# Kernel tuning notes

Measured on AMD Instinct MI355X. Metric: run time of the kernel, lower is better.

The kernel has to match this reference:

```python
import jax, jax.numpy as jnp
import numpy as np

N_NODES = 100000
N_EDGES = 1600000
D_FEAT = 64


def setup_inputs() -> dict:
    key = jax.random.key(0)
    k1, k2 = jax.random.split(key)
    x = jax.random.normal(k1, (N_NODES, D_FEAT), dtype=jnp.float32)
    edge_index = jax.random.randint(k2, (2, N_EDGES), 0, N_NODES, dtype=jnp.int64)
    alpha = jnp.ones((), dtype=jnp.float32)
    res_scale = jnp.ones((), dtype=jnp.float32)
    return {"x": x, "alpha": alpha, "res_scale": res_scale, "edge_index": edge_index}


def reference(x, alpha, res_scale, edge_index):
    """LGConv (symmetric gcn_norm, no self-loops) -> alpha-scale -> residual.

    out_i = alpha * sum_{(j->i) in E} x_j / sqrt(deg_i * deg_j) + res_scale * x_i
    """
    n = x.shape[0]
    row, col = edge_index[0], edge_index[1]  # source, target
    # degree from target index (as in PyG gcn_norm with add_self_loops=False)
    deg = jax.ops.segment_sum(jnp.ones(row.shape[0], dtype=x.dtype), col, num_segments=n)
    deg_inv_sqrt = jnp.where(deg > 0, jax.lax.rsqrt(jnp.maximum(deg, 1.0)), 0.0)
    norm = deg_inv_sqrt[row] * deg_inv_sqrt[col]  # (E,)
    msgs = norm[:, None] * x[row]                  # (E, d) gather + scale
    out = jax.ops.segment_sum(msgs, col, num_segments=n)  # scatter-add to targets
    return alpha * out + res_scale * x
```

## Files before the change

### kernel.cpp

```cpp
#include <hip/hip_runtime.h>
#include <hip/hip_bf16.h>

#define D_FEAT 64
#define OVF_CAP 65536
#define EB 8192
#define NBMAX 1024

typedef unsigned int uint32;

__device__ inline float blo(uint32 u) { return __uint_as_float(u << 16); }
__device__ inline float bhi(uint32 u) { return __uint_as_float(u & 0xffff0000u); }
__device__ inline float dinv(int d) { return (d > 0) ? rsqrtf((float)d) : 0.0f; }
__device__ inline uint32 pack_bf16x2(float a, float b) {
    __hip_bfloat16 ba = __float2bfloat16(a);
    __hip_bfloat16 bb = __float2bfloat16(b);
    uint32 ua = *reinterpret_cast<unsigned short*>(&ba);
    uint32 ub = *reinterpret_cast<unsigned short*>(&bb);
    return ua | (ub << 16);
}

__global__ __launch_bounds__(256) void k_hist(const int* __restrict__ col,
                                              int* __restrict__ histT,
                                              int E, int B, int nb) {
    __shared__ int h[NBMAX];
    for (int i = threadIdx.x; i < nb; i += 256) h[i] = 0;
    __syncthreads();
    const int b = blockIdx.x;
    const int s = b * EB;
    const int e = (s + EB < E) ? s + EB : E;
    for (int i = s + threadIdx.x; i < e; i += 256)
        atomicAdd(&h[col[i] >> 8], 1);
    __syncthreads();
    for (int k = threadIdx.x; k < nb; k += 256)
        histT[(size_t)k * B + b] = h[k];
}

__global__ __launch_bounds__(512) void k_colscan(int* __restrict__ histT,
                                                 int* __restrict__ total, int B) {
    __shared__ int sh[512];
    const int k = blockIdx.x;
    int v = (threadIdx.x < B) ? histT[(size_t)k * B + threadIdx.x] : 0;
    sh[threadIdx.x] = v;
    __syncthreads();
    for (int off = 1; off < 512; off <<= 1) {
        int t = (threadIdx.x >= off) ? sh[threadIdx.x - off] : 0;
        __syncthreads();
        sh[threadIdx.x] += t;
        __syncthreads();
    }
    int incl = sh[threadIdx.x];
    if (threadIdx.x < B) histT[(size_t)k * B + threadIdx.x] = incl - v;
    if (threadIdx.x == 511) total[k] = incl;
}

__global__ __launch_bounds__(1024) void k_tinyscan(const int* __restrict__ total,
                                                   int* __restrict__ bstart,
                                                   int* __restrict__ ovf_cnt, int nb) {
    __shared__ int sh[1024];
    int v = (threadIdx.x < nb) ? total[threadIdx.x] : 0;
    sh[threadIdx.x] = v;
    __syncthreads();
    for (int off = 1; off < 1024; off <<= 1) {
        int t = (threadIdx.x >= off) ? sh[threadIdx.x - off] : 0;
        __syncthreads();
        sh[threadIdx.x] += t;
        __syncthreads();
    }
    if (threadIdx.x < nb) bstart[threadIdx.x] = sh[threadIdx.x] - v;
    if (threadIdx.x == nb - 1) bstart[nb] = sh[threadIdx.x];
    if (threadIdx.x == 1023) *ovf_cnt = 0;
}

__global__ __launch_bounds__(256) void k_scat3(const int* __restrict__ row,
                                               const int* __restrict__ col,
                                               const int* __restrict__ histT,
                                               const int* __restrict__ bstart,
                                               uint32* __restrict__ binned,
                                               int E, int B, int nb) {
    __shared__ int cur[NBMAX];
    const int b = blockIdx.x;
    for (int k = threadIdx.x; k < nb; k += 256)
        cur[k] = bstart[k] + histT[(size_t)k * B + b];
    __syncthreads();
    const int s = b * EB;
    const int e = (s + EB < E) ? s + EB : E;
    for (int i = s + threadIdx.x; i < e; i += 256) {
        int c = col[i];
        uint32 r = (uint32)row[i];
        int pos = atomicAdd(&cur[c >> 8], 1);
        binned[pos] = (r << 8) | (uint32)(c & 255);
    }
}

__global__ __launch_bounds__(1024) void k_build(const int* __restrict__ bstart,
                                                const uint32* __restrict__ binned,
                                                const float2* __restrict__ x2,
                                                int* __restrict__ slots,
                                                int* __restrict__ deg,
                                                uint32* __restrict__ xb,
                                                int2* __restrict__ ovf,
                                                int* __restrict__ ovf_cnt,
                                                int n, int C) {
    __shared__ int cnt[256];
    __shared__ float sw[256];
    const int k = blockIdx.x;
    if (threadIdx.x < 256) cnt[threadIdx.x] = 0;
    __syncthreads();
    const int s = bstart[k], e = bstart[k + 1];
    const int base = k << 8;
    for (int i = s + threadIdx.x; i < e; i += 1024) {
        uint32 pk = binned[i];
        int cl = (int)(pk & 255);
        int r  = (int)(pk >> 8);
        int rk = atomicAdd(&cnt[cl], 1);
        int c  = base + cl;
        if (rk < C) {
            slots[(size_t)c * C + rk] = r;
        } else {
            int o = atomicAdd(ovf_cnt, 1);
            if (o < OVF_CAP) ovf[o] = make_int2(r, c);
        }
    }
    __syncthreads();
    if (threadIdx.x < 256) {
        int i = base + threadIdx.x;
        int d = cnt[threadIdx.x];
        sw[threadIdx.x] = dinv(d);
        if (i < n) deg[i] = d;
    }
    __syncthreads();
    for (int idx = threadIdx.x; idx < 256 * 32; idx += 1024) {
        int nl = idx >> 5;
        int i  = base + nl;
        if (i >= n) break;
        float w = sw[nl];
        float2 v = x2[(size_t)i * 32 + (idx & 31)];
        xb[(size_t)i * 32 + (idx & 31)] = pack_bf16x2(v.x * w, v.y * w);
    }
}

__global__ void k_gather2(const uint32* __restrict__ xb,
                          const float4* __restrict__ x4,
                          const int* __restrict__ deg,
                          const int* __restrict__ slots,
                          const float* __restrict__ alpha_p,
                          const float* __restrict__ rs_p,
                          float4* __restrict__ out4, int n, int C) {
    int wave = (blockIdx.x * blockDim.x + threadIdx.x) >> 6;
    const int lane = threadIdx.x & 63;
    const int half = lane >> 5;
    const int hl   = lane & 31;
    const int q    = hl >> 3;
    const int l    = hl & 7;
    int wid = wave * 2 + half;
    bool active = (wid < n);
    int d = active ? deg[wid] : 0;
    int e = (d < C) ? d : C;
    const int* sl = slots + (size_t)wid * C;
    float a0 = 0.f, a1 = 0.f, a2 = 0.f, a3 = 0.f;
    float a4 = 0.f, a5 = 0.f, a6 = 0.f, a7 = 0.f;
    for (int k = 0; k < e; k += 8) {
        int k1 = k + q;
        int k2 = k + 4 + q;
        if (k1 < e) {
            int s0 = sl[k1];
            uint4 p = ((const uint4*)(xb + (size_t)s0 * 32))[l];
            a0 += blo(p.x); a1 += bhi(p.x); a2 += blo(p.y); a3 += bhi(p.y);
            a4 += blo(p.z); a5 += bhi(p.z); a6 += blo(p.w); a7 += bhi(p.w);
        }
        if (k2 < e) {
            int s1 = sl[k2];
            uint4 p = ((const uint4*)(xb + (size_t)s1 * 32))[l];
            a0 += blo(p.x); a1 += bhi(p.x); a2 += blo(p.y); a3 += bhi(p.y);
            a4 += blo(p.z); a5 += bhi(p.z); a6 += blo(p.w); a7 += bhi(p.w);
        }
    }
    a0 += __shfl_down(a0, 16, 64); a1 += __shfl_down(a1, 16, 64);
    a2 += __shfl_down(a2, 16, 64); a3 += __shfl_down(a3, 16, 64);
    a4 += __shfl_down(a4, 16, 64); a5 += __shfl_down(a5, 16, 64);
    a6 += __shfl_down(a6, 16, 64); a7 += __shfl_down(a7, 16, 64);
    a0 += __shfl_down(a0, 8, 64);  a1 += __shfl_down(a1, 8, 64);
    a2 += __shfl_down(a2, 8, 64);  a3 += __shfl_down(a3, 8, 64);
    a4 += __shfl_down(a4, 8, 64);  a5 += __shfl_down(a5, 8, 64);
    a6 += __shfl_down(a6, 8, 64);  a7 += __shfl_down(a7, 8, 64);
    if (q == 0 && active) {
        float adw = (*alpha_p) * dinv(d);
        float rs  = *rs_p;
        size_t base = (size_t)wid * 16 + 2 * l;
        float4 xr0 = x4[base];
        float4 xr1 = x4[base + 1];
        float4 o0, o1;
        o0.x = fmaf(adw, a0, rs * xr0.x);
        o0.y = fmaf(adw, a1, rs * xr0.y);
        o0.z = fmaf(adw, a2, rs * xr0.z);
        o0.w = fmaf(adw, a3, rs * xr0.w);
        o1.x = fmaf(adw, a4, rs * xr1.x);
        o1.y = fmaf(adw, a5, rs * xr1.y);
        o1.z = fmaf(adw, a6, rs * xr1.z);
        o1.w = fmaf(adw, a7, rs * xr1.w);
        out4[base]     = o0;
        out4[base + 1] = o1;
    }
}

__global__ void k_ovf(const int2* __restrict__ ovf, const int* __restrict__ cnt_p,
                      const float* __restrict__ x, const int* __restrict__ deg,
                      const float* __restrict__ alpha_p, float* __restrict__ out) {
    int cnt = *cnt_p;
    if (cnt > OVF_CAP) cnt = OVF_CAP;
    if (cnt <= 0) return;
    float a = *alpha_p;
    long long total = (long long)cnt * 64;
    long long stride = (long long)gridDim.x * blockDim.x;
    for (long long idx = blockIdx.x * (long long)blockDim.x + threadIdx.x;
         idx < total; idx += stride) {
        int e = (int)(idx >> 6);
        int f = (int)(idx & 63);
        int2 rc = ovf[e];
        float w = a * dinv(deg[rc.x]) * dinv(deg[rc.y]);
        atomicAdd(&out[(size_t)rc.y * D_FEAT + f], w * x[(size_t)rc.x * D_FEAT + f]);
    }
}

__global__ void k_prep(const int* __restrict__ row, const int* __restrict__ col,
                       int* __restrict__ deg, int* __restrict__ slots,
                       int2* __restrict__ ovf, int* __restrict__ ovf_cnt,
                       int E, int C) {
    int t = blockIdx.x * blockDim.x + threadIdx.x;
    if (t < E) {
        int c = col[t];
        int r = row[t];
        int rk = atomicAdd(&deg[c], 1);
        if (rk < C) {
            slots[(size_t)c * C + rk] = r;
        } else {
            int o = atomicAdd(ovf_cnt, 1);
            if (o < OVF_CAP) ovf[o] = make_int2(r, c);
        }
    }
}
__global__ void k_cast(const float2* __restrict__ x2, const int* __restrict__ deg,
                       uint32* __restrict__ xb, int nhalf) {
    int t = blockIdx.x * blockDim.x + threadIdx.x;
    if (t < nhalf) {
        float w = dinv(deg[t >> 5]);
        float2 v = x2[t];
        xb[t] = pack_bf16x2(v.x * w, v.y * w);
    }
}

static inline char* align_up(char* p, size_t a) {
    return (char*)(((uintptr_t)p + (a - 1)) & ~(uintptr_t)(a - 1));
}

extern "C" void kernel_launch(void* const* d_in, const int* in_sizes, int n_in,
                              void* d_out, int out_size, void* d_ws, size_t ws_size,
                              hipStream_t stream) {
    const float* x         = (const float*)d_in[0];
    const float* alpha     = (const float*)d_in[1];
    const float* res_scale = (const float*)d_in[2];
    const int*   ei        = (const int*)d_in[3];

    const int n = in_sizes[0] / D_FEAT;
    const int E = in_sizes[3] / 2;
    const int* row = ei;
    const int* col = ei + E;

    float* out = (float*)d_out;
    const int nhalf = n * (D_FEAT / 2);
    const int nb = (n + 255) >> 8;
    const int B  = (E + EB - 1) / EB;

    const int nwaves = (n + 1) / 2;
    const int gblocks = (nwaves * 64 + 255) / 256;

    {
        char* p = (char*)d_ws;
        int*    deg     = (int*)p;            p += (size_t)n * 4;
        int*    ovf_cnt = (int*)p;            p += 4;
        int2*   ovf     = (int2*)p;           p += (size_t)OVF_CAP * 8;
        int*    histT   = (int*)p;            p += (size_t)nb * B * 4;
        int*    total   = (int*)p;            p += (size_t)nb * 4;
        int*    bstart  = (int*)p;            p += (size_t)(nb + 1) * 4;
        p = align_up(p, 16);
        uint32* xb      = (uint32*)p;         p += (size_t)n * 128;
        uint32* binned  = (uint32*)p;         p += (size_t)E * 4;
        int*    slots   = (int*)p;
        const size_t fixed = (size_t)(p - (char*)d_ws);

        int C = 0;
        if (ws_size > fixed) {
            size_t c_avail = (ws_size - fixed) / ((size_t)n * 4);
            C = (c_avail > 32) ? 32 : (int)c_avail;
        }
        const bool ok = (C >= 16) && (nb <= NBMAX) && (B <= 512) &&
                        (n <= (NBMAX << 8));
        if (ok) {
            k_hist    <<<B, 256, 0, stream>>>(col, histT, E, B, nb);
            k_colscan <<<nb, 512, 0, stream>>>(histT, total, B);
            k_tinyscan<<<1, 1024, 0, stream>>>(total, bstart, ovf_cnt, nb);
            k_scat3   <<<B, 256, 0, stream>>>(row, col, histT, bstart, binned,
                                              E, B, nb);
            k_build   <<<nb, 1024, 0, stream>>>(bstart, binned, (const float2*)x,
                                                slots, deg, xb, ovf, ovf_cnt, n, C);
            k_gather2<<<gblocks, 256, 0, stream>>>(xb, (const float4*)x, deg, slots,
                                                   alpha, res_scale, (float4*)out,
                                                   n, C);
            k_ovf<<<64, 256, 0, stream>>>(ovf, ovf_cnt, x, deg, alpha, out);
            return;
        }
    }

    {
        char* p = (char*)d_ws;
        int*    deg     = (int*)p;            p += (size_t)n * 4;
        int*    ovf_cnt = (int*)p;            p += 4;
        int2*   ovf     = (int2*)p;           p += (size_t)OVF_CAP * 8;
        p = align_up(p, 16);
        uint32* xb      = (uint32*)p;         p += (size_t)n * 128;
        int*    slots   = (int*)p;
        const size_t fixed = (size_t)(p - (char*)d_ws);
        int C = 0;
        if (ws_size > fixed) {
            size_t c_avail = (ws_size - fixed) / ((size_t)n * 4);
            C = (c_avail > 32) ? 32 : (int)c_avail;
        }
        if (C < 1) return;
        hipMemsetAsync(deg, 0, (size_t)n * 4 + 4, stream);
        k_prep<<<(E + 255) / 256, 256, 0, stream>>>(row, col, deg, slots,
                                                    ovf, ovf_cnt, E, C);
        k_cast<<<(nhalf + 255) / 256, 256, 0, stream>>>((const float2*)x, deg,
                                                        xb, nhalf);
        k_gather2<<<gblocks, 256, 0, stream>>>(xb, (const float4*)x, deg, slots,
                                               alpha, res_scale, (float4*)out, n, C);
        k_ovf<<<64, 256, 0, stream>>>(ovf, ovf_cnt, x, deg, alpha, out);
    }
}
```

Measured before the change: 189.6 us.

## Fuse binning pipeline stages into one cooperative kernel with grid syncs

Replaces the five-kernel CSR build (histogram, column scan, tiny scan, scatter, build) with one cooperative kernel that separates the phases with grid.sync. Grid size is max(E/8192, nb), giving 391 blocks of 512 threads for the test sizes. The goal is to remove four kernel launch gaps. In exchange it adds grid-wide barriers and depends on all 391 blocks being co-resident. The build phase now runs with 512 threads per block instead of 1024, and the old non-binned fallback path is removed.

```diff
diff --git a/kernel.cpp b/kernel.cpp
--- a/kernel.cpp
+++ b/kernel.cpp
@@ -1,5 +1,8 @@
 #include <hip/hip_runtime.h>
+#include <hip/hip_cooperative_groups.h>
 #include <hip/hip_bf16.h>
+
+namespace cg = cooperative_groups;
 
 #define D_FEAT 64
 #define OVF_CAP 65536
@@ -19,123 +22,110 @@
     return ua | (ub << 16);
 }
 
-__global__ __launch_bounds__(256) void k_hist(const int* __restrict__ col,
-                                              int* __restrict__ histT,
-                                              int E, int B, int nb) {
-    __shared__ int h[NBMAX];
-    for (int i = threadIdx.x; i < nb; i += 256) h[i] = 0;
-    __syncthreads();
+__global__ __launch_bounds__(512, 4) void k_coop(
+        const int* __restrict__ row, const int* __restrict__ col,
+        const float2* __restrict__ x2,
+        int* __restrict__ histT, int* __restrict__ total, int* __restrict__ bstart,
+        uint32* __restrict__ binned, int* __restrict__ slots,
+        int* __restrict__ deg, uint32* __restrict__ xb,
+        int2* __restrict__ ovf, int* __restrict__ ovf_cnt,
+        int n, int E, int nb, int C) {
+    cg::grid_group grid = cg::this_grid();
+    __shared__ int h[512];
+    __shared__ float sw[256];
+    const int G = gridDim.x;
     const int b = blockIdx.x;
-    const int s = b * EB;
-    const int e = (s + EB < E) ? s + EB : E;
-    for (int i = s + threadIdx.x; i < e; i += 256)
-        atomicAdd(&h[col[i] >> 8], 1);
-    __syncthreads();
-    for (int k = threadIdx.x; k < nb; k += 256)
-        histT[(size_t)k * B + b] = h[k];
-}
-
-__global__ __launch_bounds__(512) void k_colscan(int* __restrict__ histT,
-                                                 int* __restrict__ total, int B) {
-    __shared__ int sh[512];
-    const int k = blockIdx.x;
-    int v = (threadIdx.x < B) ? histT[(size_t)k * B + threadIdx.x] : 0;
-    sh[threadIdx.x] = v;
-    __syncthreads();
-    for (int off = 1; off < 512; off <<= 1) {
-        int t = (threadIdx.x >= off) ? sh[threadIdx.x - off] : 0;
-        __syncthreads();
-        sh[threadIdx.x] += t;
-        __syncthreads();
-    }
-    int incl = sh[threadIdx.x];
-    if (threadIdx.x < B) histT[(size_t)k * B + threadIdx.x] = incl - v;
-    if (threadIdx.x == 511) total[k] = incl;
-}
-
-__global__ __launch_bounds__(1024) void k_tinyscan(const int* __restrict__ total,
-                                                   int* __restrict__ bstart,
-                                                   int* __restrict__ ovf_cnt, int nb) {
-    __shared__ int sh[1024];
-    int v = (threadIdx.x < nb) ? total[threadIdx.x] : 0;
-    sh[threadIdx.x] = v;
-    __syncthreads();
-    for (int off = 1; off < 1024; off <<= 1) {
-        int t = (threadIdx.x >= off) ? sh[threadIdx.x - off] : 0;
-        __syncthreads();
-        sh[threadIdx.x] += t;
-        __syncthreads();
-    }
-    if (threadIdx.x < nb) bstart[threadIdx.x] = sh[threadIdx.x] - v;
-    if (threadIdx.x == nb - 1) bstart[nb] = sh[threadIdx.x];
-    if (threadIdx.x == 1023) *ovf_cnt = 0;
-}
-
-__global__ __launch_bounds__(256) void k_scat3(const int* __restrict__ row,
-                                               const int* __restrict__ col,
-                                               const int* __restrict__ histT,
-                                               const int* __restrict__ bstart,
-                                               uint32* __restrict__ binned,
-                                               int E, int B, int nb) {
-    __shared__ int cur[NBMAX];
-    const int b = blockIdx.x;
-    for (int k = threadIdx.x; k < nb; k += 256)
-        cur[k] = bstart[k] + histT[(size_t)k * B + b];
-    __syncthreads();
-    const int s = b * EB;
-    const int e = (s + EB < E) ? s + EB : E;
-    for (int i = s + threadIdx.x; i < e; i += 256) {
+    const int t = threadIdx.x;
+    const int EBc = (E + G - 1) / G;
+    const int s = b * EBc;
+    const int e = (s + EBc < E) ? s + EBc : E;
+
+    for (int i = t; i < nb; i += 512) h[i] = 0;
+    __syncthreads();
+    for (int i = s + t; i < e; i += 512) atomicAdd(&h[col[i] >> 8], 1);
+    __syncthreads();
+    for (int k = t; k < nb; k += 512) histT[(size_t)k * G + b] = h[k];
+    __threadfence();
+    grid.sync();
+
+    if (b < nb) {
+        int v = (t < G) ? histT[(size_t)b * G + t] : 0;
+        h[t] = v;
+        __syncthreads();
+        for (int off = 1; off < 512; off <<= 1) {
+            int u = (t >= off) ? h[t - off] : 0;
+            __syncthreads();
+            h[t] += u;
+            __syncthreads();
+        }
+        if (t < G) histT[(size_t)b * G + t] = h[t] - v;
+        if (t == 511) total[b] = h[511];
+    }
+    __threadfence();
+    grid.sync();
+
+    if (b == 0) {
+        int v = (t < nb) ? total[t] : 0;
+        h[t] = v;
+        __syncthreads();
+        for (int off = 1; off < 512; off <<= 1) {
+            int u = (t >= off) ? h[t - off] : 0;
+            __syncthreads();
+            h[t] += u;
+            __syncthreads();
+        }
+        if (t < nb) bstart[t] = h[t] - v;
+        if (t == nb - 1) bstart[nb] = h[t];
+        if (t == 0) *ovf_cnt = 0;
+    }
+    __threadfence();
+    grid.sync();
+
+    for (int k = t; k < nb; k += 512) h[k] = bstart[k] + histT[(size_t)k * G + b];
+    __syncthreads();
+    for (int i = s + t; i < e; i += 512) {
         int c = col[i];
         uint32 r = (uint32)row[i];
-        int pos = atomicAdd(&cur[c >> 8], 1);
+        int pos = atomicAdd(&h[c >> 8], 1);
         binned[pos] = (r << 8) | (uint32)(c & 255);
     }
-}
-
-__global__ __launch_bounds__(1024) void k_build(const int* __restrict__ bstart,
-                                                const uint32* __restrict__ binned,
-                                                const float2* __restrict__ x2,
-                                                int* __restrict__ slots,
-                                                int* __restrict__ deg,
-                                                uint32* __restrict__ xb,
-                                                int2* __restrict__ ovf,
-                                                int* __restrict__ ovf_cnt,
-                                                int n, int C) {
-    __shared__ int cnt[256];
-    __shared__ float sw[256];
-    const int k = blockIdx.x;
-    if (threadIdx.x < 256) cnt[threadIdx.x] = 0;
-    __syncthreads();
-    const int s = bstart[k], e = bstart[k + 1];
-    const int base = k << 8;
-    for (int i = s + threadIdx.x; i < e; i += 1024) {
-        uint32 pk = binned[i];
-        int cl = (int)(pk & 255);
-        int r  = (int)(pk >> 8);
-        int rk = atomicAdd(&cnt[cl], 1);
-        int c  = base + cl;
-        if (rk < C) {
-            slots[(size_t)c * C + rk] = r;
-        } else {
-            int o = atomicAdd(ovf_cnt, 1);
-            if (o < OVF_CAP) ovf[o] = make_int2(r, c);
-        }
-    }
-    __syncthreads();
-    if (threadIdx.x < 256) {
-        int i = base + threadIdx.x;
-        int d = cnt[threadIdx.x];
-        sw[threadIdx.x] = dinv(d);
-        if (i < n) deg[i] = d;
-    }
-    __syncthreads();
-    for (int idx = threadIdx.x; idx < 256 * 32; idx += 1024) {
-        int nl = idx >> 5;
-        int i  = base + nl;
-        if (i >= n) break;
-        float w = sw[nl];
-        float2 v = x2[(size_t)i * 32 + (idx & 31)];
-        xb[(size_t)i * 32 + (idx & 31)] = pack_bf16x2(v.x * w, v.y * w);
+    __threadfence();
+    grid.sync();
+
+    if (b < nb) {
+        if (t < 256) h[t] = 0;
+        __syncthreads();
+        const int bs = bstart[b], be = bstart[b + 1];
+        const int base = b << 8;
+        for (int i = bs + t; i < be; i += 512) {
+            uint32 pk = binned[i];
+            int cl = (int)(pk & 255);
+            int r  = (int)(pk >> 8);
+            int rk = atomicAdd(&h[cl], 1);
+            int c  = base + cl;
+            if (rk < C) {
+                slots[(size_t)c * C + rk] = r;
+            } else {
+                int o = atomicAdd(ovf_cnt, 1);
+                if (o < OVF_CAP) ovf[o] = make_int2(r, c);
+            }
+        }
+        __syncthreads();
+        if (t < 256) {
+            int i = base + t;
+            int d = h[t];
+            sw[t] = dinv(d);
+            if (i < n) deg[i] = d;
+        }
+        __syncthreads();
+        for (int idx = t; idx < 256 * 32; idx += 512) {
+            int nl = idx >> 5;
+            int i  = base + nl;
+            if (i >= n) break;
+            float w = sw[nl];
+            float2 v = x2[(size_t)i * 32 + (idx & 31)];
+            xb[(size_t)i * 32 + (idx & 31)] = pack_bf16x2(v.x * w, v.y * w);
+        }
     }
 }
 
@@ -222,15 +212,101 @@
     }
 }
 
-__global__ void k_prep(const int* __restrict__ row, const int* __restrict__ col,
-                       int* __restrict__ deg, int* __restrict__ slots,
-                       int2* __restrict__ ovf, int* __restrict__ ovf_cnt,
-                       int E, int C) {
-    int t = blockIdx.x * blockDim.x + threadIdx.x;
-    if (t < E) {
-        int c = col[t];
-        int r = row[t];
-        int rk = atomicAdd(&deg[c], 1);
+__global__ __launch_bounds__(256) void k_hist(const int* __restrict__ col,
+                                              int* __restrict__ histT,
+                                              int E, int B, int nb) {
+    __shared__ int h[NBMAX];
+    for (int i = threadIdx.x; i < nb; i += 256) h[i] = 0;
+    __syncthreads();
+    const int b = blockIdx.x;
+    const int s = b * EB;
+    const int e = (s + EB < E) ? s + EB : E;
+    for (int i = s + threadIdx.x; i < e; i += 256)
+        atomicAdd(&h[col[i] >> 8], 1);
+    __syncthreads();
+    for (int k = threadIdx.x; k < nb; k += 256)
+        histT[(size_t)k * B + b] = h[k];
+}
+
+__global__ __launch_bounds__(512) void k_colscan(int* __restrict__ histT,
+                                                 int* __restrict__ total, int B) {
+    __shared__ int sh[512];
+    const int k = blockIdx.x;
+    int v = (threadIdx.x < B) ? histT[(size_t)k * B + threadIdx.x] : 0;
+    sh[threadIdx.x] = v;
+    __syncthreads();
+    for (int off = 1; off < 512; off <<= 1) {
+        int t = (threadIdx.x >= off) ? sh[threadIdx.x - off] : 0;
+        __syncthreads();
+        sh[threadIdx.x] += t;
+        __syncthreads();
+    }
+    int incl = sh[threadIdx.x];
+    if (threadIdx.x < B) histT[(size_t)k * B + threadIdx.x] = incl - v;
+    if (threadIdx.x == 511) total[k] = incl;
+}
+
+__global__ __launch_bounds__(1024) void k_tinyscan(const int* __restrict__ total,
+                                                   int* __restrict__ bstart,
+                                                   int* __restrict__ ovf_cnt, int nb) {
+    __shared__ int sh[1024];
+    int v = (threadIdx.x < nb) ? total[threadIdx.x] : 0;
+    sh[threadIdx.x] = v;
+    __syncthreads();
+    for (int off = 1; off < 1024; off <<= 1) {
+        int t = (threadIdx.x >= off) ? sh[threadIdx.x - off] : 0;
+        __syncthreads();
+        sh[threadIdx.x] += t;
+        __syncthreads();
+    }
+    if (threadIdx.x < nb) bstart[threadIdx.x] = sh[threadIdx.x] - v;
+    if (threadIdx.x == nb - 1) bstart[nb] = sh[threadIdx.x];
+    if (threadIdx.x == 1023) *ovf_cnt = 0;
+}
+
+__global__ __launch_bounds__(256) void k_scat3(const int* __restrict__ row,
+                                               const int* __restrict__ col,
+                                               const int* __restrict__ histT,
+                                               const int* __restrict__ bstart,
+                                               uint32* __restrict__ binned,
+                                               int E, int B, int nb) {
+    __shared__ int cur[NBMAX];
+    const int b = blockIdx.x;
+    for (int k = threadIdx.x; k < nb; k += 256)
+        cur[k] = bstart[k] + histT[(size_t)k * B + b];
+    __syncthreads();
+    const int s = b * EB;
+    const int e = (s + EB < E) ? s + EB : E;
+    for (int i = s + threadIdx.x; i < e; i += 256) {
+        int c = col[i];
+        uint32 r = (uint32)row[i];
+        int pos = atomicAdd(&cur[c >> 8], 1);
+        binned[pos] = (r << 8) | (uint32)(c & 255);
+    }
+}
+
+__global__ __launch_bounds__(1024) void k_build(const int* __restrict__ bstart,
+                                                const uint32* __restrict__ binned,
+                                                const float2* __restrict__ x2,
+                                                int* __restrict__ slots,
+                                                int* __restrict__ deg,
+                                                uint32* __restrict__ xb,
+                                                int2* __restrict__ ovf,
+                                                int* __restrict__ ovf_cnt,
+                                                int n, int C) {
+    __shared__ int cnt[256];
+    __shared__ float sw[256];
+    const int k = blockIdx.x;
+    if (threadIdx.x < 256) cnt[threadIdx.x] = 0;
+    __syncthreads();
+    const int s = bstart[k], e = bstart[k + 1];
+    const int base = k << 8;
+    for (int i = s + threadIdx.x; i < e; i += 1024) {
+        uint32 pk = binned[i];
+        int cl = (int)(pk & 255);
+        int r  = (int)(pk >> 8);
+        int rk = atomicAdd(&cnt[cl], 1);
+        int c  = base + cl;
         if (rk < C) {
             slots[(size_t)c * C + rk] = r;
         } else {
@@ -238,14 +314,21 @@
             if (o < OVF_CAP) ovf[o] = make_int2(r, c);
         }
     }
-}
-__global__ void k_cast(const float2* __restrict__ x2, const int* __restrict__ deg,
-                       uint32* __restrict__ xb, int nhalf) {
-    int t = blockIdx.x * blockDim.x + threadIdx.x;
-    if (t < nhalf) {
-        float w = dinv(deg[t >> 5]);
-        float2 v = x2[t];
-        xb[t] = pack_bf16x2(v.x * w, v.y * w);
+    __syncthreads();
+    if (threadIdx.x < 256) {
+        int i = base + threadIdx.x;
+        int d = cnt[threadIdx.x];
+        sw[threadIdx.x] = dinv(d);
+        if (i < n) deg[i] = d;
+    }
+    __syncthreads();
+    for (int idx = threadIdx.x; idx < 256 * 32; idx += 1024) {
+        int nl = idx >> 5;
+        int i  = base + nl;
+        if (i >= n) break;
+        float w = sw[nl];
+        float2 v = x2[(size_t)i * 32 + (idx & 31)];
+        xb[(size_t)i * 32 + (idx & 31)] = pack_bf16x2(v.x * w, v.y * w);
     }
 }
 
@@ -261,78 +344,63 @@
     const float* res_scale = (const float*)d_in[2];
     const int*   ei        = (const int*)d_in[3];
 
-    const int n = in_sizes[0] / D_FEAT;
-    const int E = in_sizes[3] / 2;
-    const int* row = ei;
-    const int* col = ei + E;
+    int n = in_sizes[0] / D_FEAT;
+    int E = in_sizes[3] / 2;
+    const int* row = (const int*)ei;
+    const int* col = (const int*)ei + E;
 
     float* out = (float*)d_out;
-    const int nhalf = n * (D_FEAT / 2);
     const int nb = (n + 255) >> 8;
-    const int B  = (E + EB - 1) / EB;
 
     const int nwaves = (n + 1) / 2;
     const int gblocks = (nwaves * 64 + 255) / 256;
 
-    {
-        char* p = (char*)d_ws;
-        int*    deg     = (int*)p;            p += (size_t)n * 4;
-        int*    ovf_cnt = (int*)p;            p += 4;
-        int2*   ovf     = (int2*)p;           p += (size_t)OVF_CAP * 8;
-        int*    histT   = (int*)p;            p += (size_t)nb * B * 4;
-        int*    total   = (int*)p;            p += (size_t)nb * 4;
-        int*    bstart  = (int*)p;            p += (size_t)(nb + 1) * 4;
-        p = align_up(p, 16);
-        uint32* xb      = (uint32*)p;         p += (size_t)n * 128;
-        uint32* binned  = (uint32*)p;         p += (size_t)E * 4;
-        int*    slots   = (int*)p;
-        const size_t fixed = (size_t)(p - (char*)d_ws);
-
-        int C = 0;
-        if (ws_size > fixed) {
-            size_t c_avail = (ws_size - fixed) / ((size_t)n * 4);
-            C = (c_avail > 32) ? 32 : (int)c_avail;
-        }
-        const bool ok = (C >= 16) && (nb <= NBMAX) && (B <= 512) &&
-                        (n <= (NBMAX << 8));
-        if (ok) {
-            k_hist    <<<B, 256, 0, stream>>>(col, histT, E, B, nb);
-            k_colscan <<<nb, 512, 0, stream>>>(histT, total, B);
-            k_tinyscan<<<1, 1024, 0, stream>>>(total, bstart, ovf_cnt, nb);
-            k_scat3   <<<B, 256, 0, stream>>>(row, col, histT, bstart, binned,
-                                              E, B, nb);
-            k_build   <<<nb, 1024, 0, stream>>>(bstart, binned, (const float2*)x,
-                                                slots, deg, xb, ovf, ovf_cnt, n, C);
-            k_gather2<<<gblocks, 256, 0, stream>>>(xb, (const float4*)x, deg, slots,
-                                                   alpha, res_scale, (float4*)out,
-                                                   n, C);
-            k_ovf<<<64, 256, 0, stream>>>(ovf, ovf_cnt, x, deg, alpha, out);
-            return;
-        }
-    }
-
-    {
-        char* p = (char*)d_ws;
-        int*    deg     = (int*)p;            p += (size_t)n * 4;
-        int*    ovf_cnt = (int*)p;            p += 4;
-        int2*   ovf     = (int2*)p;           p += (size_t)OVF_CAP * 8;
-        p = align_up(p, 16);
-        uint32* xb      = (uint32*)p;         p += (size_t)n * 128;
-        int*    slots   = (int*)p;
-        const size_t fixed = (size_t)(p - (char*)d_ws);
-        int C = 0;
-        if (ws_size > fixed) {
-            size_t c_avail = (ws_size - fixed) / ((size_t)n * 4);
-            C = (c_avail > 32) ? 32 : (int)c_avail;
-        }
-        if (C < 1) return;
-        hipMemsetAsync(deg, 0, (size_t)n * 4 + 4, stream);
-        k_prep<<<(E + 255) / 256, 256, 0, stream>>>(row, col, deg, slots,
-                                                    ovf, ovf_cnt, E, C);
-        k_cast<<<(nhalf + 255) / 256, 256, 0, stream>>>((const float2*)x, deg,
-                                                        xb, nhalf);
-        k_gather2<<<gblocks, 256, 0, stream>>>(xb, (const float4*)x, deg, slots,
-                                               alpha, res_scale, (float4*)out, n, C);
-        k_ovf<<<64, 256, 0, stream>>>(ovf, ovf_cnt, x, deg, alpha, out);
-    }
-}
+    int Gc = (E + 8191) / 8192;
+    if (Gc < nb) Gc = nb;
+
+    const int Bfall = (E + EB - 1) / EB;
+    const int Hcols = (Gc > Bfall) ? Gc : Bfall;
+    char* p = (char*)d_ws;
+    int*    deg     = (int*)p;            p += (size_t)n * 4;
+    int*    ovf_cnt = (int*)p;            p += 4;
+    int2*   ovf     = (int2*)p;           p += (size_t)OVF_CAP * 8;
+    int*    histT   = (int*)p;            p += (size_t)nb * Hcols * 4;
+    int*    total   = (int*)p;            p += (size_t)nb * 4;
+    int*    bstart  = (int*)p;            p += (size_t)(nb + 1) * 4;
+    p = align_up(p, 16);
+    uint32* xb      = (uint32*)p;         p += (size_t)n * 128;
+    uint32* binned  = (uint32*)p;         p += (size_t)E * 4;
+    int*    slots   = (int*)p;
+    const size_t fixed = (size_t)(p - (char*)d_ws);
+
+    int C = 0;
+    if (ws_size > fixed) {
+        size_t c_avail = (ws_size - fixed) / ((size_t)n * 4);
+        C = (c_avail > 32) ? 32 : (int)c_avail;
+    }
+    if (C < 16) return;
+
+    const bool coop_ok = (nb <= 512) && (Gc <= 512);
+
+    if (coop_ok) {
+        void* args[] = {
+            (void*)&row, (void*)&col, (void*)&x, (void*)&histT, (void*)&total,
+            (void*)&bstart, (void*)&binned, (void*)&slots, (void*)&deg,
+            (void*)&xb, (void*)&ovf, (void*)&ovf_cnt,
+            (void*)&n, (void*)&E, (void*)&nb, (void*)&C };
+        hipLaunchCooperativeKernel((const void*)k_coop, dim3(Gc), dim3(512),
+                                   args, 0, stream);
+    } else {
+        k_hist    <<<Bfall, 256, 0, stream>>>(col, histT, E, Bfall, nb);
+        k_colscan <<<nb, 512, 0, stream>>>(histT, total, Bfall);
+        k_tinyscan<<<1, 1024, 0, stream>>>(total, bstart, ovf_cnt, nb);
+        k_scat3   <<<Bfall, 256, 0, stream>>>(row, col, histT, bstart, binned,
+                                              E, Bfall, nb);
+        k_build   <<<nb, 1024, 0, stream>>>(bstart, binned, (const float2*)x,
+                                            slots, deg, xb, ovf, ovf_cnt, n, C);
+    }
+
+    k_gather2<<<gblocks, 256, 0, stream>>>(xb, (const float4*)x, deg, slots,
+                                           alpha, res_scale, (float4*)out, n, C);
+    k_ovf<<<64, 256, 0, stream>>>(ovf, ovf_cnt, x, deg, alpha, out);
+}
```

Measured after the change: 639.4 us. 3.37x slower.
